# Kernel tuning notes

Hardware: AMD Instinct MI355X
Metric: run time of the kernel (lower is better)

The kernel has to match this reference:

```python
import jax, jax.numpy as jnp
import numpy as np

H, W = 2048, 2048
N_PTS = 1_000_000
N_POS = 100_000
EMB = 32

def setup_inputs() -> dict:
    key = jax.random.key(0)
    ks = jax.random.split(key, 12)
    scale = jnp.array([H, W], dtype=jnp.float32)
    x = jax.random.uniform(ks[0], (N_PTS, 2), dtype=jnp.float32) * (scale - 1.0)
    positions = jax.random.uniform(ks[1], (N_POS, 2), dtype=jnp.float32) * scale
    neighbor_map = jax.random.randint(ks[2], (H, W, 4), 0, N_POS, dtype=jnp.int32)
    embeddings = jax.random.normal(ks[3], (N_POS, EMB), dtype=jnp.float32) * 0.001
    W1 = jax.random.normal(ks[4], (64, EMB), dtype=jnp.float32) / np.sqrt(EMB)
    b1 = jax.random.normal(ks[5], (64,), dtype=jnp.float32) * 0.01
    W2 = jax.random.normal(ks[6], (64, 64), dtype=jnp.float32) / np.sqrt(64)
    b2 = jax.random.normal(ks[7], (64,), dtype=jnp.float32) * 0.01
    W3 = jax.random.normal(ks[8], (3, 64), dtype=jnp.float32) / np.sqrt(64)
    b3 = jax.random.normal(ks[9], (3,), dtype=jnp.float32) * 0.01
    mu = jax.random.uniform(ks[10], (3,), dtype=jnp.float32)
    std = jax.random.uniform(ks[11], (3,), dtype=jnp.float32) + 0.1
    return {"x": x, "positions": positions, "neighbor_map": neighbor_map,
            "embeddings": embeddings, "W1": W1, "b1": b1, "W2": W2, "b2": b2,
            "W3": W3, "b3": b3, "mu": mu, "std": std}

def reference(x, positions, neighbor_map, embeddings, W1, b1, W2, b2, W3, b3, mu, std):
    # LatentMap: floor -> neighbor gather -> distance-weighted embedding sum
    int_pos = jnp.floor(x).astype(jnp.int32)                 # [N, 2]
    nb = neighbor_map[int_pos[:, 0], int_pos[:, 1]]          # [N, 4]
    nb_pos = positions[nb]                                   # [N, 4, 2]
    diff = nb_pos - int_pos[:, None, :].astype(jnp.float32)  # [N, 4, 2]
    dist = jax.lax.stop_gradient(jnp.linalg.norm(diff, axis=-1))  # [N, 4]
    latent = jnp.einsum('nk,nkd->nd', dist, embeddings[nb])  # [N, 32]
    # tiny MLP (equinox Linear: y = x @ W.T + b), relu on hidden layers
    h = jax.nn.relu(latent @ W1.T + b1)
    h = jax.nn.relu(h @ W2.T + b2)
    out = h @ W3.T + b3                                      # [N, 3]
    # denormalize (mu/std are stop_gradient'ed in the original)
    out = out * jax.lax.stop_gradient(std) + jax.lax.stop_gradient(mu)
    # NaN-guarded clip: per-point cond(any NaN -> mu, else clip to [0,1])
    has_nan = jnp.any(jnp.isnan(out), axis=-1, keepdims=True)
    return jnp.where(has_nan, jax.lax.stop_gradient(mu), jnp.clip(out, 0.0, 1.0))
```

## Files before the change

kernel.cpp:

```cpp
#include <hip/hip_runtime.h>
#include <hip/hip_bf16.h>


typedef __attribute__((ext_vector_type(2))) float f32x2;
typedef __attribute__((ext_vector_type(4))) float f32x4;
typedef __attribute__((ext_vector_type(4))) int   i32x4;
typedef __attribute__((ext_vector_type(8))) short s16x8;
typedef __attribute__((ext_vector_type(4))) _Float16 f16x4;

#define GRID_W  2048
#define LSTR    36
#define PSTR    68
#define SEL_HI  0x05040100u
#define SEL_LO  0x07060302u
#define LGKM0   0xC07F

static __device__ __forceinline__ unsigned bits_bf2(__hip_bfloat162 h) {
    union { __hip_bfloat162 b; unsigned u; } cv; cv.b = h; return cv.u;
}
static __device__ __forceinline__ void split2_packed(float v0, float v1, unsigned &p0, unsigned &p1) {
    float2 f; f.x = v0; f.y = v1;
    unsigned hu = bits_bf2(__float22bfloat162_rn(f));
    float2 d;
    d.x = v0 - __uint_as_float(hu << 16);
    d.y = v1 - __uint_as_float(hu & 0xffff0000u);
    unsigned lu = bits_bf2(__float22bfloat162_rn(d));
    p0 = (hu & 0xffffu) | (lu << 16);
    p1 = (hu >> 16) | (lu & 0xffff0000u);
}
static __device__ __forceinline__ s16x8 unpack8(uint4 q0, uint4 q1, unsigned sel) {
    union { unsigned u[4]; s16x8 v; } r;
    r.u[0] = __builtin_amdgcn_perm(q0.y, q0.x, sel);
    r.u[1] = __builtin_amdgcn_perm(q0.w, q0.z, sel);
    r.u[2] = __builtin_amdgcn_perm(q1.y, q1.x, sel);
    r.u[3] = __builtin_amdgcn_perm(q1.w, q1.z, sel);
    return r.v;
}
static __device__ __forceinline__ s16x8 load_wbf(const float* p) {
    f32x4 a = ((const f32x4*)p)[0];
    f32x4 b = ((const f32x4*)p)[1];
    union { unsigned u[4]; s16x8 v; } r;
    float2 f;
    f.x = a.x; f.y = a.y; r.u[0] = bits_bf2(__float22bfloat162_rn(f));
    f.x = a.z; f.y = a.w; r.u[1] = bits_bf2(__float22bfloat162_rn(f));
    f.x = b.x; f.y = b.y; r.u[2] = bits_bf2(__float22bfloat162_rn(f));
    f.x = b.z; f.y = b.w; r.u[3] = bits_bf2(__float22bfloat162_rn(f));
    return r.v;
}
static __device__ __forceinline__ void lds_fence() {
    __builtin_amdgcn_wave_barrier();
    __builtin_amdgcn_s_waitcnt(LGKM0);
    __builtin_amdgcn_wave_barrier();
}

__global__ __launch_bounds__(256) void emb_cast_f16(
    const float* __restrict__ in, _Float16* __restrict__ out, int n4)
{
    int i = blockIdx.x * blockDim.x + threadIdx.x;
    int stride = gridDim.x * blockDim.x;
    for (; i < n4; i += stride) {
        f32x4 v = ((const f32x4*)in)[i];
        f16x4 o;
        o.x = (_Float16)v.x; o.y = (_Float16)v.y;
        o.z = (_Float16)v.z; o.w = (_Float16)v.w;
        ((f16x4*)out)[i] = o;
    }
}

template <bool F16>
__global__ __launch_bounds__(256, 2) void fused_persistent(
    const float* __restrict__ x,
    const float* __restrict__ positions,
    const int*   __restrict__ nbmap,
    const void*  __restrict__ embp,
    const float* __restrict__ W1,
    const float* __restrict__ b1,
    const float* __restrict__ W2,
    const float* __restrict__ b2,
    const float* __restrict__ W3,
    const float* __restrict__ b3,
    const float* __restrict__ mu,
    const float* __restrict__ sd,
    float* __restrict__ out,
    int npts)
{
    const int tid  = threadIdx.x;
    const int w    = tid >> 6;
    const int lid  = tid & 63;
    const int quad = lid >> 4;
    const int m16  = lid & 15;
    const int c8   = lid & 7;
    const int pr   = lid >> 3;

    const int nwav = gridDim.x * 4;
    const int wgid = blockIdx.x * 4 + w;
    const int NCH  = (npts + 31) >> 5;
    if (wgid >= NCH) return;

    __shared__ __align__(16) unsigned lat_lds[4 * 32 * LSTR];
    unsigned* latw = lat_lds + w * 32 * LSTR;
    unsigned* hb   = latw;

    const f32x2* Xv  = (const f32x2*)x;
    const f32x2* Pv  = (const f32x2*)positions;
    const i32x4* NBq = (const i32x4*)nbmap;

    s16x8 w1f[4];
#pragma unroll
    for (int nt = 0; nt < 4; ++nt)
        w1f[nt] = load_wbf(W1 + (nt * 16 + m16) * 32 + quad * 8);
    s16x8 w2f[2][4];
#pragma unroll
    for (int s = 0; s < 2; ++s)
#pragma unroll
        for (int nt = 0; nt < 4; ++nt)
            w2f[s][nt] = load_wbf(W2 + (nt * 16 + m16) * 64 + s * 32 + quad * 8);
    s16x8 w3f[2];
#pragma unroll
    for (int s = 0; s < 2; ++s) {
        if (m16 < 3) {
            w3f[s] = load_wbf(W3 + m16 * 64 + s * 32 + quad * 8);
        } else {
            s16x8 z = {0, 0, 0, 0, 0, 0, 0, 0};
            w3f[s] = z;
        }
    }
    float b1v[4], b2v[4];
#pragma unroll
    for (int nt = 0; nt < 4; ++nt) { b1v[nt] = b1[nt * 16 + m16]; b2v[nt] = b2[nt * 16 + m16]; }
    const int mm = (m16 < 3) ? m16 : 0;
    const float b3m = b3[mm], sdm = sd[mm], mum = mu[mm];

    f32x2 xv[4], xvn[4];
    i32x4 nb[4], nbn[4];
#pragma unroll
    for (int p = 0; p < 4; ++p) {
        int g = wgid * 32 + p * 8 + pr;
        g = (g < npts) ? g : (npts - 1);
        xv[p] = Xv[g];
    }
#pragma unroll
    for (int p = 0; p < 4; ++p) {
        int i0 = (int)xv[p].x, i1 = (int)xv[p].y;
        nb[p] = NBq[i0 * GRID_W + i1];
    }

    for (int c = wgid; c < NCH; c += nwav) {
        const int cn = c + nwav;
        const bool hn = (cn < NCH);

        if (hn) {
#pragma unroll
            for (int p = 0; p < 4; ++p) {
                int g = cn * 32 + p * 8 + pr;
                g = (g < npts) ? g : (npts - 1);
                xvn[p] = Xv[g];
            }
        }

#pragma unroll
        for (int p = 0; p < 4; ++p) {
            f32x2 xvp = xv[p];
            float f0 = (float)(int)xvp.x, f1 = (float)(int)xvp.y;
            i32x4 n4 = nb[p];
            int ids[4] = {n4.x, n4.y, n4.z, n4.w};
            float a0 = 0.f, a1 = 0.f, a2 = 0.f, a3 = 0.f;
#pragma unroll
            for (int k = 0; k < 4; ++k) {
                f32x2 pp = Pv[ids[k]];
                float dx = pp.x - f0, dy = pp.y - f1;
                float dist = sqrtf(dx * dx + dy * dy);
                float e0, e1, e2, e3;
                if constexpr (F16) {
                    const _Float16* E = (const _Float16*)embp;
                    f16x4 e = *(const f16x4*)(E + ids[k] * 32 + c8 * 4);
                    e0 = (float)e.x; e1 = (float)e.y; e2 = (float)e.z; e3 = (float)e.w;
                } else {
                    const float* E = (const float*)embp;
                    f32x4 e = *(const f32x4*)(E + ids[k] * 32 + c8 * 4);
                    e0 = e.x; e1 = e.y; e2 = e.z; e3 = e.w;
                }
                a0 = fmaf(dist, e0, a0); a1 = fmaf(dist, e1, a1);
                a2 = fmaf(dist, e2, a2); a3 = fmaf(dist, e3, a3);
            }
            unsigned p0, p1, p2, p3;
            split2_packed(a0, a1, p0, p1);
            split2_packed(a2, a3, p2, p3);
            uint4 pv; pv.x = p0; pv.y = p1; pv.z = p2; pv.w = p3;
            *(uint4*)(latw + (p * 8 + pr) * LSTR + c8 * 4) = pv;
        }
        lds_fence();

        s16x8 AH[2], AL[2];
#pragma unroll
        for (int t = 0; t < 2; ++t) {
            const unsigned* ap = latw + (t * 16 + m16) * LSTR + quad * 8;
            uint4 q0 = *(const uint4*)ap;
            uint4 q1 = *(const uint4*)(ap + 4);
            AH[t] = unpack8(q0, q1, SEL_HI);
            AL[t] = unpack8(q0, q1, SEL_LO);
        }
        lds_fence();

        if (hn) {
#pragma unroll
            for (int p = 0; p < 4; ++p) {
                int i0 = (int)xvn[p].x, i1 = (int)xvn[p].y;
                nbn[p] = NBq[i0 * GRID_W + i1];
            }
        }

#pragma unroll
        for (int t = 0; t < 2; ++t) {
            s16x8 ah = AH[t], al = AL[t];
            f32x4 c1[4];
#pragma unroll
            for (int nt = 0; nt < 4; ++nt) {
                f32x4 cc = {0.f, 0.f, 0.f, 0.f};
                cc = __builtin_amdgcn_mfma_f32_16x16x32_bf16(al, w1f[nt], cc, 0, 0, 0);
                cc = __builtin_amdgcn_mfma_f32_16x16x32_bf16(ah, w1f[nt], cc, 0, 0, 0);
                c1[nt] = cc;
            }
            __builtin_amdgcn_wave_barrier();
#pragma unroll
            for (int nt = 0; nt < 4; ++nt)
#pragma unroll
                for (int r = 0; r < 4; r += 2) {
                    float v0 = fmaxf(c1[nt][r]     + b1v[nt], 0.f);
                    float v1 = fmaxf(c1[nt][r + 1] + b1v[nt], 0.f);
                    unsigned p0, p1; split2_packed(v0, v1, p0, p1);
                    hb[(quad * 4 + r)     * PSTR + nt * 16 + m16] = p0;
                    hb[(quad * 4 + r + 1) * PSTR + nt * 16 + m16] = p1;
                }
            lds_fence();

            f32x4 c2[4] = {{0.f,0.f,0.f,0.f},{0.f,0.f,0.f,0.f},{0.f,0.f,0.f,0.f},{0.f,0.f,0.f,0.f}};
#pragma unroll
            for (int s = 0; s < 2; ++s) {
                const unsigned* rp = hb + m16 * PSTR + s * 32 + quad * 8;
                uint4 h0 = *(const uint4*)rp;
                uint4 h1 = *(const uint4*)(rp + 4);
                s16x8 a2h = unpack8(h0, h1, SEL_HI);
                s16x8 a2l = unpack8(h0, h1, SEL_LO);
#pragma unroll
                for (int nt = 0; nt < 4; ++nt) {
                    c2[nt] = __builtin_amdgcn_mfma_f32_16x16x32_bf16(a2l, w2f[s][nt], c2[nt], 0, 0, 0);
                    c2[nt] = __builtin_amdgcn_mfma_f32_16x16x32_bf16(a2h, w2f[s][nt], c2[nt], 0, 0, 0);
                }
            }
            lds_fence();
#pragma unroll
            for (int nt = 0; nt < 4; ++nt)
#pragma unroll
                for (int r = 0; r < 4; r += 2) {
                    float v0 = fmaxf(c2[nt][r]     + b2v[nt], 0.f);
                    float v1 = fmaxf(c2[nt][r + 1] + b2v[nt], 0.f);
                    unsigned p0, p1; split2_packed(v0, v1, p0, p1);
                    hb[(quad * 4 + r)     * PSTR + nt * 16 + m16] = p0;
                    hb[(quad * 4 + r + 1) * PSTR + nt * 16 + m16] = p1;
                }
            lds_fence();

            f32x4 c3 = {0.f, 0.f, 0.f, 0.f};
#pragma unroll
            for (int s = 0; s < 2; ++s) {
                const unsigned* rp = hb + m16 * PSTR + s * 32 + quad * 8;
                uint4 h0 = *(const uint4*)rp;
                uint4 h1 = *(const uint4*)(rp + 4);
                s16x8 a3h = unpack8(h0, h1, SEL_HI);
                s16x8 a3l = unpack8(h0, h1, SEL_LO);
                c3 = __builtin_amdgcn_mfma_f32_16x16x32_bf16(a3l, w3f[s], c3, 0, 0, 0);
                c3 = __builtin_amdgcn_mfma_f32_16x16x32_bf16(a3h, w3f[s], c3, 0, 0, 0);
            }
            lds_fence();
#pragma unroll
            for (int r = 0; r < 4; ++r) {
                float v = (c3[r] + b3m) * sdm + mum;
                v = fminf(fmaxf(v, 0.f), 1.f);
                int gpt = c * 32 + t * 16 + quad * 4 + r;
                if (m16 < 3 && gpt < npts) out[(size_t)gpt * 3 + m16] = v;
            }
        }

        if (hn) {
#pragma unroll
            for (int p = 0; p < 4; ++p) { xv[p] = xvn[p]; nb[p] = nbn[p]; }
        }
    }
}

extern "C" void kernel_launch(void* const* d_in, const int* in_sizes, int n_in,
                              void* d_out, int out_size, void* d_ws, size_t ws_size,
                              hipStream_t stream) {
    const float* x         = (const float*)d_in[0];
    const float* positions = (const float*)d_in[1];
    const int*   nbmap     = (const int*)d_in[2];
    const float* emb       = (const float*)d_in[3];
    const float* W1        = (const float*)d_in[4];
    const float* b1        = (const float*)d_in[5];
    const float* W2        = (const float*)d_in[6];
    const float* b2        = (const float*)d_in[7];
    const float* W3        = (const float*)d_in[8];
    const float* b3        = (const float*)d_in[9];
    const float* mu        = (const float*)d_in[10];
    const float* sd        = (const float*)d_in[11];
    float* out = (float*)d_out;

    int npts   = in_sizes[0] / 2;
    int n_embf = in_sizes[3];
    size_t need = (size_t)n_embf * sizeof(_Float16);

    int nch = (npts + 31) / 32;
    int blocks = 1024;
    int maxb = (nch + 3) / 4;
    if (blocks > maxb) blocks = maxb;

    if (d_ws != nullptr && ws_size >= need && (n_embf % 4) == 0) {
        _Float16* emb16 = (_Float16*)d_ws;
        int n4 = n_embf / 4;
        int cblocks = (n4 + 255) / 256;
        if (cblocks > 1024) cblocks = 1024;
        emb_cast_f16<<<cblocks, 256, 0, stream>>>(emb, emb16, n4);
        fused_persistent<true><<<blocks, 256, 0, stream>>>(x, positions, nbmap, emb16,
                                                           W1, b1, W2, b2, W3, b3, mu, sd,
                                                           out, npts);
    } else {
        fused_persistent<false><<<blocks, 256, 0, stream>>>(x, positions, nbmap, emb,
                                                            W1, b1, W2, b2, W3, b3, mu, sd,
                                                            out, npts);
    }
}
```

Before: 238.8 us.

## Stage W1/W2 MFMA fragments in LDS to raise occupancy

W1 and W2 bf16 weight fragments are no longer held in registers for the whole kernel. The first wave of each block writes them into shared memory once, and every MFMA step reads its fragment from LDS. This frees VGPRs, so launch bounds rise from 2 to 5 blocks per SIMD-unit target and the persistent grid grows from 1024 to 1280 blocks, giving more latency hiding for the random gathers. The cost is extra LDS reads inside the MLP inner loop, a block-wide barrier at startup, and a larger LDS footprint per block.

```diff
diff --git a/kernel.cpp b/kernel.cpp
--- a/kernel.cpp
+++ b/kernel.cpp
@@ -11,6 +11,8 @@
 #define GRID_W  2048
 #define LSTR    36
 #define PSTR    68
+#define W2OFF   (4 * 32 * LSTR)
+#define W1OFF   (W2OFF + 2048)
 #define SEL_HI  0x05040100u
 #define SEL_LO  0x07060302u
 #define LGKM0   0xC07F
@@ -68,7 +70,7 @@
 }
 
 template <bool F16>
-__global__ __launch_bounds__(256, 2) void fused_persistent(
+__global__ __launch_bounds__(256, 5) void fused_persistent(
     const float* __restrict__ x,
     const float* __restrict__ positions,
     const int*   __restrict__ nbmap,
@@ -95,26 +97,36 @@
     const int nwav = gridDim.x * 4;
     const int wgid = blockIdx.x * 4 + w;
     const int NCH  = (npts + 31) >> 5;
-    if (wgid >= NCH) return;
-
-    __shared__ __align__(16) unsigned lat_lds[4 * 32 * LSTR];
+
+    __shared__ __align__(16) unsigned lat_lds[W1OFF + 1024];
     unsigned* latw = lat_lds + w * 32 * LSTR;
     unsigned* hb   = latw;
+    unsigned* w2b  = lat_lds + W2OFF;
+    unsigned* w1b  = lat_lds + W1OFF;
+
+    if (w == 0) {
+#pragma unroll
+        for (int s = 0; s < 2; ++s)
+#pragma unroll
+            for (int nt = 0; nt < 4; ++nt) {
+                union { s16x8 v; uint4 q; } cv;
+                cv.v = load_wbf(W2 + (nt * 16 + m16) * 64 + s * 32 + quad * 8);
+                *(uint4*)(w2b + ((s * 4 + nt) * 64 + lid) * 4) = cv.q;
+            }
+#pragma unroll
+        for (int nt = 0; nt < 4; ++nt) {
+            union { s16x8 v; uint4 q; } cv;
+            cv.v = load_wbf(W1 + (nt * 16 + m16) * 32 + quad * 8);
+            *(uint4*)(w1b + (nt * 64 + lid) * 4) = cv.q;
+        }
+    }
+    __syncthreads();
+    if (wgid >= NCH) return;
 
     const f32x2* Xv  = (const f32x2*)x;
     const f32x2* Pv  = (const f32x2*)positions;
     const i32x4* NBq = (const i32x4*)nbmap;
 
-    s16x8 w1f[4];
-#pragma unroll
-    for (int nt = 0; nt < 4; ++nt)
-        w1f[nt] = load_wbf(W1 + (nt * 16 + m16) * 32 + quad * 8);
-    s16x8 w2f[2][4];
-#pragma unroll
-    for (int s = 0; s < 2; ++s)
-#pragma unroll
-        for (int nt = 0; nt < 4; ++nt)
-            w2f[s][nt] = load_wbf(W2 + (nt * 16 + m16) * 64 + s * 32 + quad * 8);
     s16x8 w3f[2];
 #pragma unroll
     for (int s = 0; s < 2; ++s) {
@@ -216,9 +228,11 @@
             f32x4 c1[4];
 #pragma unroll
             for (int nt = 0; nt < 4; ++nt) {
+                union { uint4 q; s16x8 v; } wc;
+                wc.q = *(const uint4*)(w1b + (nt * 64 + lid) * 4);
                 f32x4 cc = {0.f, 0.f, 0.f, 0.f};
-                cc = __builtin_amdgcn_mfma_f32_16x16x32_bf16(al, w1f[nt], cc, 0, 0, 0);
-                cc = __builtin_amdgcn_mfma_f32_16x16x32_bf16(ah, w1f[nt], cc, 0, 0, 0);
+                cc = __builtin_amdgcn_mfma_f32_16x16x32_bf16(al, wc.v, cc, 0, 0, 0);
+                cc = __builtin_amdgcn_mfma_f32_16x16x32_bf16(ah, wc.v, cc, 0, 0, 0);
                 c1[nt] = cc;
             }
             __builtin_amdgcn_wave_barrier();
@@ -244,8 +258,10 @@
                 s16x8 a2l = unpack8(h0, h1, SEL_LO);
 #pragma unroll
                 for (int nt = 0; nt < 4; ++nt) {
-                    c2[nt] = __builtin_amdgcn_mfma_f32_16x16x32_bf16(a2l, w2f[s][nt], c2[nt], 0, 0, 0);
-                    c2[nt] = __builtin_amdgcn_mfma_f32_16x16x32_bf16(a2h, w2f[s][nt], c2[nt], 0, 0, 0);
+                    union { uint4 q; s16x8 v; } wc;
+                    wc.q = *(const uint4*)(w2b + ((s * 4 + nt) * 64 + lid) * 4);
+                    c2[nt] = __builtin_amdgcn_mfma_f32_16x16x32_bf16(a2l, wc.v, c2[nt], 0, 0, 0);
+                    c2[nt] = __builtin_amdgcn_mfma_f32_16x16x32_bf16(a2h, wc.v, c2[nt], 0, 0, 0);
                 }
             }
             lds_fence();
@@ -311,7 +327,7 @@
     size_t need = (size_t)n_embf * sizeof(_Float16);
 
     int nch = (npts + 31) / 32;
-    int blocks = 1024;
+    int blocks = 1280;
     int maxb = (nch + 3) / 4;
     if (blocks > maxb) blocks = maxb;
 
```

After: 216.5 us. 9.3% less time.
